# Performance work log

Measured on AMD Instinct MI355X. Metric: run time of the kernel, lower is better.

Reference implementation:

```python
import jax, jax.numpy as jnp
import numpy as np

NUM_THETAS = 64   # bump_steps == num_thetas == 64
NUM_PTS = 100
B = 256           # number of graphs
N = B * NUM_PTS   # total nodes
SCALE = 500.0     # sigmoid sharpness used by EctLayer
HID = 4 * 1024


def _linear_init(key, fan_in, shape):
    s = 1.0 / np.sqrt(fan_in)
    return jax.random.uniform(key, shape, jnp.float32, -s, s)


def setup_inputs() -> dict:
    key = jax.random.key(0)
    ks = jax.random.split(key, 8)
    x = jax.random.normal(ks[0], (N, 2), jnp.float32)
    batch_idx = jnp.repeat(jnp.arange(B), NUM_PTS)  # [N] graph id per node
    t = jnp.linspace(0.0, 2.0 * np.pi, NUM_THETAS)
    V = jnp.stack([jnp.sin(t), jnp.cos(t)], axis=0)          # [2, T] directions
    lin = jnp.linspace(-1.0, 1.0, NUM_THETAS)                # [bump] thresholds
    d = NUM_THETAS * NUM_THETAS
    W1 = _linear_init(ks[1], d, (d, HID)); b1 = _linear_init(ks[2], d, (HID,))
    W2 = _linear_init(ks[3], HID, (HID, HID)); b2 = _linear_init(ks[4], HID, (HID,))
    W3 = _linear_init(ks[5], HID, (HID, 2 * NUM_PTS)); b3 = _linear_init(ks[6], HID, (2 * NUM_PTS,))
    return {"x": x, "batch_idx": batch_idx, "V": V, "lin": lin,
            "W1": W1, "b1": b1, "W2": W2, "b2": b2, "W3": W3, "b3": b3}


def ect_layer(x, idx, V, lin, num_graphs):
    # x: [N,2], V: [2,T] -> node heights nh: [N,T]
    nh = x @ V
    # soft-threshold binning: [N, bump, T]
    ecc = jax.nn.sigmoid(SCALE * (lin[None, :, None] - nh[:, None, :]))
    # per-graph scatter-sum over nodes -> [B, bump, T]
    e = jax.ops.segment_sum(ecc, idx, num_segments=num_graphs)
    # normalized=True: divide by per-graph max
    return e / jnp.amax(e, axis=(1, 2), keepdims=True)


def reference(x, batch_idx, V, lin, W1, b1, W2, b2, W3, b3):
    ect = ect_layer(x, batch_idx, V, lin, B)          # [B, 64, 64]
    h = ect.reshape(B, -1)                            # Flatten
    h = jnp.tanh(h @ W1 + b1)
    h = jnp.tanh(h @ W2 + b2)
    pts = (h @ W3 + b3).reshape(-1, 2)                # [B*NUM_PTS, 2]
    idx2 = jnp.repeat(jnp.arange(B), NUM_PTS)
    decoded = ect_layer(pts, idx2, V, lin, B)         # [B, 64, 64]
    return decoded, pts
```

## Files before the change

### kernel.cpp

```cpp
#include <hip/hip_runtime.h>
#include <hip/hip_bf16.h>

typedef short bf16x8 __attribute__((ext_vector_type(8)));
typedef short s16x4 __attribute__((ext_vector_type(4)));
typedef float f32x4 __attribute__((ext_vector_type(4)));
typedef unsigned u32x4 __attribute__((ext_vector_type(4)));

#define ECT_SCALE 500.0f

__device__ __forceinline__ bool detect_f32(const void* w) {
    const unsigned* p = (const unsigned*)w;
    int sane = 0;
#pragma unroll
    for (int i = 0; i < 16; i++) {
        unsigned e = (p[i] >> 7) & 0xFFu;
        sane += (e >= 100u && e <= 140u) ? 1 : 0;
    }
    return sane < 10;
}

__device__ __forceinline__ float ld_f(const void* p, int i, bool f32) {
    return f32 ? ((const float*)p)[i]
               : __bfloat162float(((const __hip_bfloat16*)p)[i]);
}

__device__ __forceinline__ void split_f(float v, short& hi, short& lo) {
    __hip_bfloat16 h = __float2bfloat16(v);
    hi = (short)__bfloat16_as_short(h);
    lo = (short)__bfloat16_as_short(__float2bfloat16(v - __bfloat162float(h)));
}

__device__ __forceinline__ float sig_fast(float x) {
    float t = __builtin_amdgcn_fmed3f(x, 0.0f, 1.0f);
    return t * t * (3.0f - 2.0f * t);
}

__global__ __launch_bounds__(512)
void ect1_kernel(const void* __restrict__ x, const void* __restrict__ V,
                 const void* __restrict__ lin, const void* __restrict__ sent,
                 short* __restrict__ eh, short* __restrict__ el)
{
    __shared__ float in_lds[200];
    __shared__ float nh[100 * 64];
    __shared__ float wmax[8];

    const bool f32 = detect_f32(sent);
    const int g = blockIdx.x, tid = threadIdx.x;
    const int t = tid & 63, wv = tid >> 6;

    if (tid < 200) in_lds[tid] = ld_f(x, g * 200 + tid, f32);
    const float sv = ld_f(V, t, f32);
    const float cv = ld_f(V, 64 + t, f32);
    float zs[8];
#pragma unroll
    for (int k = 0; k < 8; k++)
        zs[k] = (ECT_SCALE / 8.0f) * ld_f(lin, wv + 8 * k, f32) + 0.5f;
    __syncthreads();

    for (int n = wv; n < 100; n += 8)
        nh[n * 64 + t] = in_lds[2 * n] * sv + in_lds[2 * n + 1] * cv;

    float e[8];
#pragma unroll
    for (int k = 0; k < 8; k++) e[k] = 0.0f;
    __syncthreads();

    for (int n = 0; n < 100; n++) {
        const float ws = (ECT_SCALE / 8.0f) * nh[n * 64 + t];
#pragma unroll
        for (int k = 0; k < 8; k++)
            e[k] += sig_fast(zs[k] - ws);
    }

    float mx = e[0];
#pragma unroll
    for (int k = 1; k < 8; k++) mx = fmaxf(mx, e[k]);
#pragma unroll
    for (int off = 32; off > 0; off >>= 1)
        mx = fmaxf(mx, __shfl_xor(mx, off, 64));
    if (t == 0) wmax[wv] = mx;
    __syncthreads();
    float gm = wmax[0];
#pragma unroll
    for (int k = 1; k < 8; k++) gm = fmaxf(gm, wmax[k]);
    const float sc = 1.0f / gm;

#pragma unroll
    for (int k = 0; k < 8; k++) {
        short hi, lo;
        split_f(e[k] * sc, hi, lo);
        eh[g * 4096 + tid + 512 * k] = hi;
        el[g * 4096 + tid + 512 * k] = lo;
    }
}

#define PREFETCH(k0_)                                                          \
    {                                                                          \
        _Pragma("unroll")                                                      \
        for (int p = 0; p < 2; p++) {                                          \
            int r = ar + 64 * p;                                               \
            pah[p] = *(const bf16x8*)&Ah[(size_t)(bm * 128 + r) * 4096 + (k0_) + ac]; \
            pal[p] = *(const bf16x8*)&Al[(size_t)(bm * 128 + r) * 4096 + (k0_) + ac]; \
        }                                                                      \
        _Pragma("unroll")                                                      \
        for (int c = 0; c < 2; c++)                                            \
            _Pragma("unroll")                                                  \
            for (int j = 0; j < 8; j++) {                                      \
                size_t off = (size_t)((k0_) + wk + j) * 4096 + n0c + lane + 64 * c; \
                pw[c * 8 + j] = f32 ? ((const unsigned*)W)[off]                \
                                    : ((unsigned)((const unsigned short*)W)[off] << 16); \
            }                                                                  \
    }

__global__ __launch_bounds__(256)
void gemm128(const short* __restrict__ Ah, const short* __restrict__ Al,
             const void* __restrict__ W, const void* __restrict__ sent,
             float* __restrict__ pre)
{
    __shared__ short Ahs[128][40], Als[128][40], Bhs[128][40], Bls[128][40];
    const bool f32 = detect_f32(sent);
    const int bm = blockIdx.y;
    const int bn = blockIdx.x >> 3;
    const int kz = blockIdx.x & 7;
    const int tid = threadIdx.x;
    const int wv = tid >> 6, lane = tid & 63, quad = lane >> 4, l16 = lane & 15;
    const int wm = (wv & 1) * 64, wn = (wv >> 1) * 64;
    const int ar = tid >> 2, ac = (tid & 3) * 8;
    const int n0c = bn * 128;
    const int wk = wv * 8;

    f32x4 acc[4][4];
#pragma unroll
    for (int i = 0; i < 4; i++)
#pragma unroll
        for (int j = 0; j < 4; j++) acc[i][j] = (f32x4){0.f, 0.f, 0.f, 0.f};

    bf16x8 pah[2], pal[2];
    unsigned pw[16];

    const int k0base = kz * 512;
    PREFETCH(k0base)

    for (int it = 0; it < 16; it++) {
#pragma unroll
        for (int p = 0; p < 2; p++) {
            *(bf16x8*)&Ahs[ar + 64 * p][ac] = pah[p];
            *(bf16x8*)&Als[ar + 64 * p][ac] = pal[p];
        }
#pragma unroll
        for (int c = 0; c < 2; c++) {
            unsigned hp[4], lp[4];
#pragma unroll
            for (int jp = 0; jp < 4; jp++) {
                unsigned a = pw[c * 8 + 2 * jp], b = pw[c * 8 + 2 * jp + 1];
                unsigned ha = a & 0xFFFF0000u, hb = b & 0xFFFF0000u;
                hp[jp] = (ha >> 16) | hb;
                float la = __uint_as_float(a) - __uint_as_float(ha);
                float lb = __uint_as_float(b) - __uint_as_float(hb);
                lp[jp] = (__float_as_uint(la) >> 16) |
                         (__float_as_uint(lb) & 0xFFFF0000u);
            }
            *(u32x4*)&Bhs[lane + 64 * c][wk] = (u32x4){hp[0], hp[1], hp[2], hp[3]};
            *(u32x4*)&Bls[lane + 64 * c][wk] = (u32x4){lp[0], lp[1], lp[2], lp[3]};
        }
        __syncthreads();

        if (it < 15) PREFETCH(k0base + (it + 1) * 32)

        bf16x8 ahf[4], alf[4];
#pragma unroll
        for (int i = 0; i < 4; i++) {
            ahf[i] = *(const bf16x8*)&Ahs[wm + i * 16 + l16][quad * 8];
            alf[i] = *(const bf16x8*)&Als[wm + i * 16 + l16][quad * 8];
        }
#pragma unroll
        for (int j = 0; j < 4; j++) {
            bf16x8 bh = *(const bf16x8*)&Bhs[wn + j * 16 + l16][quad * 8];
            bf16x8 bl = *(const bf16x8*)&Bls[wn + j * 16 + l16][quad * 8];
#pragma unroll
            for (int i = 0; i < 4; i++) {
                acc[i][j] = __builtin_amdgcn_mfma_f32_16x16x32_bf16(ahf[i], bh, acc[i][j], 0, 0, 0);
                acc[i][j] = __builtin_amdgcn_mfma_f32_16x16x32_bf16(ahf[i], bl, acc[i][j], 0, 0, 0);
                acc[i][j] = __builtin_amdgcn_mfma_f32_16x16x32_bf16(alf[i], bh, acc[i][j], 0, 0, 0);
            }
        }
        __syncthreads();
    }

    float* ps = pre + (size_t)kz * (256 * 4096);
#pragma unroll
    for (int i = 0; i < 4; i++)
#pragma unroll
        for (int j = 0; j < 4; j++) {
            const int n = n0c + wn + j * 16 + l16;
#pragma unroll
            for (int r = 0; r < 4; r++) {
                const int m = bm * 128 + wm + i * 16 + quad * 4 + r;
                ps[(size_t)m * 4096 + n] = acc[i][j][r];
            }
        }
}

__global__ __launch_bounds__(256)
void finalize8(const float* __restrict__ pre, const void* __restrict__ bias,
               const void* __restrict__ sent,
               short* __restrict__ Oh, short* __restrict__ Ol)
{
    const bool f32 = detect_f32(sent);
    const int idx = (blockIdx.x * 256 + threadIdx.x) * 4;
    f32x4 s = (f32x4){0.f, 0.f, 0.f, 0.f};
#pragma unroll
    for (int z = 0; z < 8; z++)
        s += *(const f32x4*)&pre[(size_t)z * 1048576 + idx];
    const int n = idx & 4095;
    s16x4 hi, lo;
#pragma unroll
    for (int j = 0; j < 4; j++) {
        float t = s[j] + ld_f(bias, n + j, f32);
        t = 1.0f - 2.0f * __builtin_amdgcn_rcpf(1.0f + __expf(2.0f * t));
        short h, l;
        split_f(t, h, l);
        hi[j] = h; lo[j] = l;
    }
    *(s16x4*)&Oh[idx] = hi;
    *(s16x4*)&Ol[idx] = lo;
}

__global__ __launch_bounds__(256)
void gemm_sk3(const short* __restrict__ Ah, const short* __restrict__ Al,
              const void* __restrict__ W, const void* __restrict__ sent,
              float* __restrict__ part)
{
    __shared__ short Ahs[64][72], Als[64][72], Bhs[64][72], Bls[64][72];
    const bool f32 = detect_f32(sent);
    const int N_ = 200, K_ = 4096;
    const int bm = blockIdx.y;
    const int bn = blockIdx.x >> 5;
    const int kz = blockIdx.x & 31;
    const int tid = threadIdx.x;
    const int wv = tid >> 6, lane = tid & 63, quad = lane >> 4, l16 = lane & 15;
    const int mrow0 = (wv & 1) * 32, ncol0 = (wv >> 1) * 32;
    const int rr = tid >> 3, cc = (tid & 7) * 8;
    const int n0c = bn * 64;

    f32x4 acc[2][2];
#pragma unroll
    for (int i = 0; i < 2; i++)
#pragma unroll
        for (int j = 0; j < 2; j++) acc[i][j] = (f32x4){0.f, 0.f, 0.f, 0.f};

    int k0 = kz * 128;
    for (int it = 0; it < 2; it++, k0 += 64) {
#pragma unroll
        for (int i = 0; i < 2; i++) {
            int r = rr + 32 * i;
            *(bf16x8*)&Ahs[r][cc] = *(const bf16x8*)&Ah[(size_t)(bm * 64 + r) * K_ + k0 + cc];
            *(bf16x8*)&Als[r][cc] = *(const bf16x8*)&Al[(size_t)(bm * 64 + r) * K_ + k0 + cc];
        }
        {
            const int wn2 = lane, wk2 = wv * 16;
            const bool okn = (n0c + wn2 < N_);
            unsigned pw2[16];
#pragma unroll
            for (int j = 0; j < 16; j++) {
                size_t off = (size_t)(k0 + wk2 + j) * N_ + n0c + wn2;
                pw2[j] = !okn ? 0u
                       : (f32 ? ((const unsigned*)W)[off]
                              : ((unsigned)((const unsigned short*)W)[off] << 16));
            }
            unsigned hp[8], lp[8];
#pragma unroll
            for (int jp = 0; jp < 8; jp++) {
                unsigned a = pw2[2 * jp], b = pw2[2 * jp + 1];
                unsigned ha = a & 0xFFFF0000u, hb = b & 0xFFFF0000u;
                hp[jp] = (ha >> 16) | hb;
                float la = __uint_as_float(a) - __uint_as_float(ha);
                float lb = __uint_as_float(b) - __uint_as_float(hb);
                lp[jp] = (__float_as_uint(la) >> 16) | (__float_as_uint(lb) & 0xFFFF0000u);
            }
            *(u32x4*)&Bhs[wn2][wk2]     = (u32x4){hp[0], hp[1], hp[2], hp[3]};
            *(u32x4*)&Bhs[wn2][wk2 + 8] = (u32x4){hp[4], hp[5], hp[6], hp[7]};
            *(u32x4*)&Bls[wn2][wk2]     = (u32x4){lp[0], lp[1], lp[2], lp[3]};
            *(u32x4*)&Bls[wn2][wk2 + 8] = (u32x4){lp[4], lp[5], lp[6], lp[7]};
        }
        __syncthreads();
#pragma unroll
        for (int kh = 0; kh < 2; kh++) {
            bf16x8 ah2[2], al2[2];
#pragma unroll
            for (int im = 0; im < 2; im++) {
                ah2[im] = *(const bf16x8*)&Ahs[mrow0 + im * 16 + l16][kh * 32 + quad * 8];
                al2[im] = *(const bf16x8*)&Als[mrow0 + im * 16 + l16][kh * 32 + quad * 8];
            }
#pragma unroll
            for (int jn = 0; jn < 2; jn++) {
                bf16x8 bh = *(const bf16x8*)&Bhs[ncol0 + jn * 16 + l16][kh * 32 + quad * 8];
                bf16x8 bl = *(const bf16x8*)&Bls[ncol0 + jn * 16 + l16][kh * 32 + quad * 8];
#pragma unroll
                for (int im = 0; im < 2; im++) {
                    acc[im][jn] = __builtin_amdgcn_mfma_f32_16x16x32_bf16(ah2[im], bh, acc[im][jn], 0, 0, 0);
                    acc[im][jn] = __builtin_amdgcn_mfma_f32_16x16x32_bf16(ah2[im], bl, acc[im][jn], 0, 0, 0);
                    acc[im][jn] = __builtin_amdgcn_mfma_f32_16x16x32_bf16(al2[im], bh, acc[im][jn], 0, 0, 0);
                }
            }
        }
        __syncthreads();
    }

    float* ps = part + (size_t)kz * (256 * 200);
#pragma unroll
    for (int im = 0; im < 2; im++)
#pragma unroll
        for (int jn = 0; jn < 2; jn++) {
            const int n = n0c + ncol0 + jn * 16 + l16;
            if (n < N_) {
#pragma unroll
                for (int r = 0; r < 4; r++) {
                    const int m = bm * 64 + mrow0 + im * 16 + quad * 4 + r;
                    ps[m * 200 + n] = acc[im][jn][r];
                }
            }
        }
}

__global__ __launch_bounds__(512)
void ect2_kernel(const float* __restrict__ part, const void* __restrict__ bias3,
                 const void* __restrict__ V, const void* __restrict__ lin,
                 const void* __restrict__ sent,
                 float* __restrict__ dec, float* __restrict__ pts_out)
{
    __shared__ float in_lds[200];
    __shared__ float nh[100 * 64];
    __shared__ float wmax[8];

    const bool f32 = detect_f32(sent);
    const int g = blockIdx.x, tid = threadIdx.x;
    const int t = tid & 63, wv = tid >> 6;

    if (tid < 200) {
        float v = ld_f(bias3, tid, f32);
#pragma unroll
        for (int z = 0; z < 32; z++)
            v += part[(size_t)z * 51200 + g * 200 + tid];
        in_lds[tid] = v;
        pts_out[g * 200 + tid] = v;
    }
    const float sv = ld_f(V, t, f32);
    const float cv = ld_f(V, 64 + t, f32);
    float zs[8];
#pragma unroll
    for (int k = 0; k < 8; k++)
        zs[k] = (ECT_SCALE / 8.0f) * ld_f(lin, wv + 8 * k, f32) + 0.5f;
    __syncthreads();

    for (int n = wv; n < 100; n += 8)
        nh[n * 64 + t] = in_lds[2 * n] * sv + in_lds[2 * n + 1] * cv;

    float e[8];
#pragma unroll
    for (int k = 0; k < 8; k++) e[k] = 0.0f;
    __syncthreads();

    for (int n = 0; n < 100; n++) {
        const float ws = (ECT_SCALE / 8.0f) * nh[n * 64 + t];
#pragma unroll
        for (int k = 0; k < 8; k++)
            e[k] += sig_fast(zs[k] - ws);
    }

    float mx = e[0];
#pragma unroll
    for (int k = 1; k < 8; k++) mx = fmaxf(mx, e[k]);
#pragma unroll
    for (int off = 32; off > 0; off >>= 1)
        mx = fmaxf(mx, __shfl_xor(mx, off, 64));
    if (t == 0) wmax[wv] = mx;
    __syncthreads();
    float gm = wmax[0];
#pragma unroll
    for (int k = 1; k < 8; k++) gm = fmaxf(gm, wmax[k]);
    const float sc = 1.0f / gm;

#pragma unroll
    for (int k = 0; k < 8; k++)
        dec[g * 4096 + tid + 512 * k] = e[k] * sc;
}

extern "C" void kernel_launch(void* const* d_in, const int* in_sizes, int n_in,
                              void* d_out, int out_size, void* d_ws, size_t ws_size,
                              hipStream_t stream)
{
    const void* x   = d_in[0];
    const void* V   = d_in[2];
    const void* lin = d_in[3];
    const void* W1  = d_in[4];
    const void* b1  = d_in[5];
    const void* W2  = d_in[6];
    const void* b2  = d_in[7];
    const void* W3  = d_in[8];
    const void* b3  = d_in[9];
    float* out = (float*)d_out;

    char* ws = (char*)d_ws;
    short* e_h  = (short*)(ws + ( 0u << 20));
    short* e_l  = (short*)(ws + ( 2u << 20));
    short* h1h  = (short*)(ws + ( 4u << 20));
    short* h1l  = (short*)(ws + ( 6u << 20));
    short* h2h  = (short*)(ws + ( 8u << 20));
    short* h2l  = (short*)(ws + (10u << 20));
    float* pre  = (float*)(ws + (12u << 20));
    float* part = (float*)(ws + (44u << 20));

    ect1_kernel<<<256, 512, 0, stream>>>(x, V, lin, W1, e_h, e_l);
    gemm128<<<dim3(256, 2), 256, 0, stream>>>(e_h, e_l, W1, W1, pre);
    finalize8<<<1024, 256, 0, stream>>>(pre, b1, W1, h1h, h1l);
    gemm128<<<dim3(256, 2), 256, 0, stream>>>(h1h, h1l, W2, W1, pre);
    finalize8<<<1024, 256, 0, stream>>>(pre, b2, W1, h2h, h2l);
    gemm_sk3<<<dim3(128, 4), 256, 0, stream>>>(h2h, h2l, W3, W1, part);
    ect2_kernel<<<256, 512, 0, stream>>>(part, b3, V, lin, W1, out, out + 1048576);
}
```

Baseline: 268.9 us.

## Shrink gemm128 N-tile to 64, swizzle B LDS, skip low-part MFMAs for bf16 weights

The gemm128 N-tile drops from 128 to 64 columns and the grid doubles, so more blocks are resident (launch bounds now request 4 per CU) and each wave holds fewer accumulators. B-tile LDS writes and reads use an XOR swizzle to cut bank conflicts. Pointer-increment prefetching replaces recomputed offsets. When the weights are bf16, the low-part B split and its MFMA are skipped in both GEMM kernels, since that part is zero. The smaller tile means less reuse of each loaded A tile and more global traffic for A.

```diff
diff --git a/kernel.cpp b/kernel.cpp
--- a/kernel.cpp
+++ b/kernel.cpp
@@ -94,109 +94,132 @@
     }
 }
 
-#define PREFETCH(k0_)                                                          \
+#define STAGE_PF()                                                             \
     {                                                                          \
-        _Pragma("unroll")                                                      \
-        for (int p = 0; p < 2; p++) {                                          \
-            int r = ar + 64 * p;                                               \
-            pah[p] = *(const bf16x8*)&Ah[(size_t)(bm * 128 + r) * 4096 + (k0_) + ac]; \
-            pal[p] = *(const bf16x8*)&Al[(size_t)(bm * 128 + r) * 4096 + (k0_) + ac]; \
+        pah[0] = *(const bf16x8*)a0; pah[1] = *(const bf16x8*)a1;              \
+        pal[0] = *(const bf16x8*)l0; pal[1] = *(const bf16x8*)l1;              \
+        if (f32) {                                                             \
+            _Pragma("unroll")                                                  \
+            for (int j = 0; j < 8; j++)                                        \
+                pw[j] = *(const unsigned*)(wp + (size_t)j * wrow);             \
+        } else {                                                               \
+            _Pragma("unroll")                                                  \
+            for (int j = 0; j < 8; j++)                                        \
+                pw[j] = (unsigned)(*(const unsigned short*)(wp + (size_t)j * wrow)) << 16; \
         }                                                                      \
-        _Pragma("unroll")                                                      \
-        for (int c = 0; c < 2; c++)                                            \
-            _Pragma("unroll")                                                  \
-            for (int j = 0; j < 8; j++) {                                      \
-                size_t off = (size_t)((k0_) + wk + j) * 4096 + n0c + lane + 64 * c; \
-                pw[c * 8 + j] = f32 ? ((const unsigned*)W)[off]                \
-                                    : ((unsigned)((const unsigned short*)W)[off] << 16); \
-            }                                                                  \
-    }
-
-__global__ __launch_bounds__(256)
+        a0 += 32; a1 += 32; l0 += 32; l1 += 32; wp += 32 * wrow;               \
+    }
+
+__global__ __launch_bounds__(256, 4)
 void gemm128(const short* __restrict__ Ah, const short* __restrict__ Al,
              const void* __restrict__ W, const void* __restrict__ sent,
              float* __restrict__ pre)
 {
-    __shared__ short Ahs[128][40], Als[128][40], Bhs[128][40], Bls[128][40];
+    __shared__ short Ahs[128][40], Als[128][40], Bhs[64][40], Bls[64][40];
     const bool f32 = detect_f32(sent);
     const int bm = blockIdx.y;
     const int bn = blockIdx.x >> 3;
     const int kz = blockIdx.x & 7;
     const int tid = threadIdx.x;
     const int wv = tid >> 6, lane = tid & 63, quad = lane >> 4, l16 = lane & 15;
-    const int wm = (wv & 1) * 64, wn = (wv >> 1) * 64;
+    const int wm = wv * 32;
     const int ar = tid >> 2, ac = (tid & 3) * 8;
-    const int n0c = bn * 128;
+    const int n0c = bn * 64;
     const int wk = wv * 8;
-
-    f32x4 acc[4][4];
-#pragma unroll
-    for (int i = 0; i < 4; i++)
+    const int bwcol = (wv ^ ((lane >> 3) & 3)) * 8;
+
+    f32x4 acc[2][4];
+#pragma unroll
+    for (int i = 0; i < 2; i++)
 #pragma unroll
         for (int j = 0; j < 4; j++) acc[i][j] = (f32x4){0.f, 0.f, 0.f, 0.f};
 
     bf16x8 pah[2], pal[2];
-    unsigned pw[16];
-
-    const int k0base = kz * 512;
-    PREFETCH(k0base)
+    unsigned pw[8];
+
+    const size_t welt = f32 ? 4u : 2u;
+    const size_t wrow = (size_t)4096 * welt;
+    const char* wp = (const char*)W + ((size_t)(kz * 512 + wk) * 4096 + (n0c + lane)) * welt;
+    const short* a0 = Ah + (size_t)(bm * 128 + ar) * 4096 + kz * 512 + ac;
+    const short* a1 = a0 + (size_t)64 * 4096;
+    const short* l0 = Al + (size_t)(bm * 128 + ar) * 4096 + kz * 512 + ac;
+    const short* l1 = l0 + (size_t)64 * 4096;
+
+    STAGE_PF()
 
     for (int it = 0; it < 16; it++) {
-#pragma unroll
-        for (int p = 0; p < 2; p++) {
-            *(bf16x8*)&Ahs[ar + 64 * p][ac] = pah[p];
-            *(bf16x8*)&Als[ar + 64 * p][ac] = pal[p];
-        }
-#pragma unroll
-        for (int c = 0; c < 2; c++) {
+        *(bf16x8*)&Ahs[ar][ac]      = pah[0];
+        *(bf16x8*)&Ahs[ar + 64][ac] = pah[1];
+        *(bf16x8*)&Als[ar][ac]      = pal[0];
+        *(bf16x8*)&Als[ar + 64][ac] = pal[1];
+        {
             unsigned hp[4], lp[4];
 #pragma unroll
             for (int jp = 0; jp < 4; jp++) {
-                unsigned a = pw[c * 8 + 2 * jp], b = pw[c * 8 + 2 * jp + 1];
+                unsigned a = pw[2 * jp], b = pw[2 * jp + 1];
                 unsigned ha = a & 0xFFFF0000u, hb = b & 0xFFFF0000u;
                 hp[jp] = (ha >> 16) | hb;
-                float la = __uint_as_float(a) - __uint_as_float(ha);
-                float lb = __uint_as_float(b) - __uint_as_float(hb);
-                lp[jp] = (__float_as_uint(la) >> 16) |
-                         (__float_as_uint(lb) & 0xFFFF0000u);
-            }
-            *(u32x4*)&Bhs[lane + 64 * c][wk] = (u32x4){hp[0], hp[1], hp[2], hp[3]};
-            *(u32x4*)&Bls[lane + 64 * c][wk] = (u32x4){lp[0], lp[1], lp[2], lp[3]};
+                if (f32) {
+                    float la = __uint_as_float(a) - __uint_as_float(ha);
+                    float lb = __uint_as_float(b) - __uint_as_float(hb);
+                    lp[jp] = (__float_as_uint(la) >> 16) |
+                             (__float_as_uint(lb) & 0xFFFF0000u);
+                }
+            }
+            *(u32x4*)&Bhs[lane][bwcol] = (u32x4){hp[0], hp[1], hp[2], hp[3]};
+            if (f32)
+                *(u32x4*)&Bls[lane][bwcol] = (u32x4){lp[0], lp[1], lp[2], lp[3]};
         }
         __syncthreads();
 
-        if (it < 15) PREFETCH(k0base + (it + 1) * 32)
-
-        bf16x8 ahf[4], alf[4];
-#pragma unroll
-        for (int i = 0; i < 4; i++) {
-            ahf[i] = *(const bf16x8*)&Ahs[wm + i * 16 + l16][quad * 8];
-            alf[i] = *(const bf16x8*)&Als[wm + i * 16 + l16][quad * 8];
-        }
+        if (it < 15) STAGE_PF()
+
+        bf16x8 ahf[2], alf[2];
+#pragma unroll
+        for (int im = 0; im < 2; im++) {
+            ahf[im] = *(const bf16x8*)&Ahs[wm + im * 16 + l16][quad * 8];
+            alf[im] = *(const bf16x8*)&Als[wm + im * 16 + l16][quad * 8];
+        }
+        if (f32) {
+#pragma unroll
+            for (int j = 0; j < 4; j++) {
+                const int br = j * 16 + l16;
+                const int bc = (quad ^ ((br >> 3) & 3)) * 8;
+                bf16x8 bh = *(const bf16x8*)&Bhs[br][bc];
+                bf16x8 bl = *(const bf16x8*)&Bls[br][bc];
+#pragma unroll
+                for (int im = 0; im < 2; im++) {
+                    acc[im][j] = __builtin_amdgcn_mfma_f32_16x16x32_bf16(ahf[im], bh, acc[im][j], 0, 0, 0);
+                    acc[im][j] = __builtin_amdgcn_mfma_f32_16x16x32_bf16(ahf[im], bl, acc[im][j], 0, 0, 0);
+                    acc[im][j] = __builtin_amdgcn_mfma_f32_16x16x32_bf16(alf[im], bh, acc[im][j], 0, 0, 0);
+                }
+            }
+        } else {
+#pragma unroll
+            for (int j = 0; j < 4; j++) {
+                const int br = j * 16 + l16;
+                const int bc = (quad ^ ((br >> 3) & 3)) * 8;
+                bf16x8 bh = *(const bf16x8*)&Bhs[br][bc];
+#pragma unroll
+                for (int im = 0; im < 2; im++) {
+                    acc[im][j] = __builtin_amdgcn_mfma_f32_16x16x32_bf16(ahf[im], bh, acc[im][j], 0, 0, 0);
+                    acc[im][j] = __builtin_amdgcn_mfma_f32_16x16x32_bf16(alf[im], bh, acc[im][j], 0, 0, 0);
+                }
+            }
+        }
+        __syncthreads();
+    }
+
+    float* ps = pre + (size_t)kz * (256 * 4096);
+#pragma unroll
+    for (int im = 0; im < 2; im++)
 #pragma unroll
         for (int j = 0; j < 4; j++) {
-            bf16x8 bh = *(const bf16x8*)&Bhs[wn + j * 16 + l16][quad * 8];
-            bf16x8 bl = *(const bf16x8*)&Bls[wn + j * 16 + l16][quad * 8];
-#pragma unroll
-            for (int i = 0; i < 4; i++) {
-                acc[i][j] = __builtin_amdgcn_mfma_f32_16x16x32_bf16(ahf[i], bh, acc[i][j], 0, 0, 0);
-                acc[i][j] = __builtin_amdgcn_mfma_f32_16x16x32_bf16(ahf[i], bl, acc[i][j], 0, 0, 0);
-                acc[i][j] = __builtin_amdgcn_mfma_f32_16x16x32_bf16(alf[i], bh, acc[i][j], 0, 0, 0);
-            }
-        }
-        __syncthreads();
-    }
-
-    float* ps = pre + (size_t)kz * (256 * 4096);
-#pragma unroll
-    for (int i = 0; i < 4; i++)
-#pragma unroll
-        for (int j = 0; j < 4; j++) {
-            const int n = n0c + wn + j * 16 + l16;
+            const int n = n0c + j * 16 + l16;
 #pragma unroll
             for (int r = 0; r < 4; r++) {
-                const int m = bm * 128 + wm + i * 16 + quad * 4 + r;
-                ps[(size_t)m * 4096 + n] = acc[i][j][r];
+                const int m = bm * 128 + wm + im * 16 + quad * 4 + r;
+                ps[(size_t)m * 4096 + n] = acc[im][j][r];
             }
         }
 }
@@ -274,14 +297,18 @@
                 unsigned a = pw2[2 * jp], b = pw2[2 * jp + 1];
                 unsigned ha = a & 0xFFFF0000u, hb = b & 0xFFFF0000u;
                 hp[jp] = (ha >> 16) | hb;
-                float la = __uint_as_float(a) - __uint_as_float(ha);
-                float lb = __uint_as_float(b) - __uint_as_float(hb);
-                lp[jp] = (__float_as_uint(la) >> 16) | (__float_as_uint(lb) & 0xFFFF0000u);
+                if (f32) {
+                    float la = __uint_as_float(a) - __uint_as_float(ha);
+                    float lb = __uint_as_float(b) - __uint_as_float(hb);
+                    lp[jp] = (__float_as_uint(la) >> 16) | (__float_as_uint(lb) & 0xFFFF0000u);
+                }
             }
             *(u32x4*)&Bhs[wn2][wk2]     = (u32x4){hp[0], hp[1], hp[2], hp[3]};
             *(u32x4*)&Bhs[wn2][wk2 + 8] = (u32x4){hp[4], hp[5], hp[6], hp[7]};
-            *(u32x4*)&Bls[wn2][wk2]     = (u32x4){lp[0], lp[1], lp[2], lp[3]};
-            *(u32x4*)&Bls[wn2][wk2 + 8] = (u32x4){lp[4], lp[5], lp[6], lp[7]};
+            if (f32) {
+                *(u32x4*)&Bls[wn2][wk2]     = (u32x4){lp[0], lp[1], lp[2], lp[3]};
+                *(u32x4*)&Bls[wn2][wk2 + 8] = (u32x4){lp[4], lp[5], lp[6], lp[7]};
+            }
         }
         __syncthreads();
 #pragma unroll
@@ -292,15 +319,27 @@
                 ah2[im] = *(const bf16x8*)&Ahs[mrow0 + im * 16 + l16][kh * 32 + quad * 8];
                 al2[im] = *(const bf16x8*)&Als[mrow0 + im * 16 + l16][kh * 32 + quad * 8];
             }
-#pragma unroll
-            for (int jn = 0; jn < 2; jn++) {
-                bf16x8 bh = *(const bf16x8*)&Bhs[ncol0 + jn * 16 + l16][kh * 32 + quad * 8];
-                bf16x8 bl = *(const bf16x8*)&Bls[ncol0 + jn * 16 + l16][kh * 32 + quad * 8];
-#pragma unroll
-                for (int im = 0; im < 2; im++) {
-                    acc[im][jn] = __builtin_amdgcn_mfma_f32_16x16x32_bf16(ah2[im], bh, acc[im][jn], 0, 0, 0);
-                    acc[im][jn] = __builtin_amdgcn_mfma_f32_16x16x32_bf16(ah2[im], bl, acc[im][jn], 0, 0, 0);
-                    acc[im][jn] = __builtin_amdgcn_mfma_f32_16x16x32_bf16(al2[im], bh, acc[im][jn], 0, 0, 0);
+            if (f32) {
+#pragma unroll
+                for (int jn = 0; jn < 2; jn++) {
+                    bf16x8 bh = *(const bf16x8*)&Bhs[ncol0 + jn * 16 + l16][kh * 32 + quad * 8];
+                    bf16x8 bl = *(const bf16x8*)&Bls[ncol0 + jn * 16 + l16][kh * 32 + quad * 8];
+#pragma unroll
+                    for (int im = 0; im < 2; im++) {
+                        acc[im][jn] = __builtin_amdgcn_mfma_f32_16x16x32_bf16(ah2[im], bh, acc[im][jn], 0, 0, 0);
+                        acc[im][jn] = __builtin_amdgcn_mfma_f32_16x16x32_bf16(ah2[im], bl, acc[im][jn], 0, 0, 0);
+                        acc[im][jn] = __builtin_amdgcn_mfma_f32_16x16x32_bf16(al2[im], bh, acc[im][jn], 0, 0, 0);
+                    }
+                }
+            } else {
+#pragma unroll
+                for (int jn = 0; jn < 2; jn++) {
+                    bf16x8 bh = *(const bf16x8*)&Bhs[ncol0 + jn * 16 + l16][kh * 32 + quad * 8];
+#pragma unroll
+                    for (int im = 0; im < 2; im++) {
+                        acc[im][jn] = __builtin_amdgcn_mfma_f32_16x16x32_bf16(ah2[im], bh, acc[im][jn], 0, 0, 0);
+                        acc[im][jn] = __builtin_amdgcn_mfma_f32_16x16x32_bf16(al2[im], bh, acc[im][jn], 0, 0, 0);
+                    }
                 }
             }
         }
@@ -412,9 +451,9 @@
     float* part = (float*)(ws + (44u << 20));
 
     ect1_kernel<<<256, 512, 0, stream>>>(x, V, lin, W1, e_h, e_l);
-    gemm128<<<dim3(256, 2), 256, 0, stream>>>(e_h, e_l, W1, W1, pre);
+    gemm128<<<dim3(512, 2), 256, 0, stream>>>(e_h, e_l, W1, W1, pre);
     finalize8<<<1024, 256, 0, stream>>>(pre, b1, W1, h1h, h1l);
-    gemm128<<<dim3(256, 2), 256, 0, stream>>>(h1h, h1l, W2, W1, pre);
+    gemm128<<<dim3(512, 2), 256, 0, stream>>>(h1h, h1l, W2, W1, pre);
     finalize8<<<1024, 256, 0, stream>>>(pre, b2, W1, h2h, h2l);
     gemm_sk3<<<dim3(128, 4), 256, 0, stream>>>(h2h, h2l, W3, W1, part);
     ect2_kernel<<<256, 512, 0, stream>>>(part, b3, V, lin, W1, out, out + 1048576);
```

Result: slower. 278.5 us (+3.6%).

## Double-buffer GEMM prefetch registers and skip low-part MFMA for bf16 weights

Applied to the files above, without the earlier changes.

The main GEMM now keeps two register prefetch sets, so global loads are issued two K-steps ahead, and it walks incrementing pointers instead of recomputing addresses each step. Launch bounds ask for two blocks per CU. When the weights are detected as bf16, the low-half split, its shared-memory store and the third MFMA product are skipped in both the main GEMM and the output GEMM, because the low half is zero in that case. The cost is higher register pressure from the doubled prefetch buffers and the occupancy hint, which could cause spills.

```diff
diff --git a/kernel.cpp b/kernel.cpp
--- a/kernel.cpp
+++ b/kernel.cpp
@@ -94,25 +94,86 @@
     }
 }
 
-#define PREFETCH(k0_)                                                          \
+#define PFSET(S)                                                               \
     {                                                                          \
-        _Pragma("unroll")                                                      \
-        for (int p = 0; p < 2; p++) {                                          \
-            int r = ar + 64 * p;                                               \
-            pah[p] = *(const bf16x8*)&Ah[(size_t)(bm * 128 + r) * 4096 + (k0_) + ac]; \
-            pal[p] = *(const bf16x8*)&Al[(size_t)(bm * 128 + r) * 4096 + (k0_) + ac]; \
-        }                                                                      \
-        _Pragma("unroll")                                                      \
-        for (int c = 0; c < 2; c++)                                            \
+        pah##S[0] = *(const bf16x8*)a0; pah##S[1] = *(const bf16x8*)a1;        \
+        pal##S[0] = *(const bf16x8*)l0; pal##S[1] = *(const bf16x8*)l1;        \
+        if (f32) {                                                             \
             _Pragma("unroll")                                                  \
             for (int j = 0; j < 8; j++) {                                      \
-                size_t off = (size_t)((k0_) + wk + j) * 4096 + n0c + lane + 64 * c; \
-                pw[c * 8 + j] = f32 ? ((const unsigned*)W)[off]                \
-                                    : ((unsigned)((const unsigned short*)W)[off] << 16); \
+                pw##S[j]     = *(const unsigned*)(wp + (size_t)j * wrow);      \
+                pw##S[8 + j] = *(const unsigned*)(wp + (size_t)j * wrow + 256);\
             }                                                                  \
-    }
-
-__global__ __launch_bounds__(256)
+        } else {                                                               \
+            _Pragma("unroll")                                                  \
+            for (int j = 0; j < 8; j++) {                                      \
+                pw##S[j]     = (unsigned)(*(const unsigned short*)(wp + (size_t)j * wrow)) << 16; \
+                pw##S[8 + j] = (unsigned)(*(const unsigned short*)(wp + (size_t)j * wrow + 128)) << 16; \
+            }                                                                  \
+        }                                                                      \
+        a0 += 32; a1 += 32; l0 += 32; l1 += 32; wp += 32 * wrow;               \
+    }
+
+#define GBODY(S, IT)                                                           \
+    {                                                                          \
+        *(bf16x8*)&Ahs[ar][ac]      = pah##S[0];                               \
+        *(bf16x8*)&Ahs[ar + 64][ac] = pah##S[1];                               \
+        *(bf16x8*)&Als[ar][ac]      = pal##S[0];                               \
+        *(bf16x8*)&Als[ar + 64][ac] = pal##S[1];                               \
+        _Pragma("unroll")                                                      \
+        for (int c = 0; c < 2; c++) {                                          \
+            unsigned hp[4], lp[4];                                             \
+            _Pragma("unroll")                                                  \
+            for (int jp = 0; jp < 4; jp++) {                                   \
+                unsigned a = pw##S[c * 8 + 2 * jp], b = pw##S[c * 8 + 2 * jp + 1]; \
+                unsigned ha = a & 0xFFFF0000u, hb = b & 0xFFFF0000u;           \
+                hp[jp] = (ha >> 16) | hb;                                      \
+                if (f32) {                                                     \
+                    float la = __uint_as_float(a) - __uint_as_float(ha);       \
+                    float lb = __uint_as_float(b) - __uint_as_float(hb);       \
+                    lp[jp] = (__float_as_uint(la) >> 16) |                     \
+                             (__float_as_uint(lb) & 0xFFFF0000u);              \
+                }                                                              \
+            }                                                                  \
+            *(u32x4*)&Bhs[lane + 64 * c][wk] = (u32x4){hp[0], hp[1], hp[2], hp[3]}; \
+            if (f32)                                                           \
+                *(u32x4*)&Bls[lane + 64 * c][wk] = (u32x4){lp[0], lp[1], lp[2], lp[3]}; \
+        }                                                                      \
+        __syncthreads();                                                       \
+        if ((IT) + 2 < 16) PFSET(S)                                            \
+        bf16x8 ahf[4], alf[4];                                                 \
+        _Pragma("unroll")                                                      \
+        for (int i = 0; i < 4; i++) {                                          \
+            ahf[i] = *(const bf16x8*)&Ahs[wm + i * 16 + l16][quad * 8];        \
+            alf[i] = *(const bf16x8*)&Als[wm + i * 16 + l16][quad * 8];        \
+        }                                                                      \
+        if (f32) {                                                             \
+            _Pragma("unroll")                                                  \
+            for (int j = 0; j < 4; j++) {                                      \
+                bf16x8 bh = *(const bf16x8*)&Bhs[wn + j * 16 + l16][quad * 8]; \
+                bf16x8 bl = *(const bf16x8*)&Bls[wn + j * 16 + l16][quad * 8]; \
+                _Pragma("unroll")                                              \
+                for (int i = 0; i < 4; i++) {                                  \
+                    acc[i][j] = __builtin_amdgcn_mfma_f32_16x16x32_bf16(ahf[i], bh, acc[i][j], 0, 0, 0); \
+                    acc[i][j] = __builtin_amdgcn_mfma_f32_16x16x32_bf16(ahf[i], bl, acc[i][j], 0, 0, 0); \
+                    acc[i][j] = __builtin_amdgcn_mfma_f32_16x16x32_bf16(alf[i], bh, acc[i][j], 0, 0, 0); \
+                }                                                              \
+            }                                                                  \
+        } else {                                                               \
+            _Pragma("unroll")                                                  \
+            for (int j = 0; j < 4; j++) {                                      \
+                bf16x8 bh = *(const bf16x8*)&Bhs[wn + j * 16 + l16][quad * 8]; \
+                _Pragma("unroll")                                              \
+                for (int i = 0; i < 4; i++) {                                  \
+                    acc[i][j] = __builtin_amdgcn_mfma_f32_16x16x32_bf16(ahf[i], bh, acc[i][j], 0, 0, 0); \
+                    acc[i][j] = __builtin_amdgcn_mfma_f32_16x16x32_bf16(alf[i], bh, acc[i][j], 0, 0, 0); \
+                }                                                              \
+            }                                                                  \
+        }                                                                      \
+        __syncthreads();                                                       \
+    }
+
+__global__ __launch_bounds__(256, 2)
 void gemm128(const short* __restrict__ Ah, const short* __restrict__ Al,
              const void* __restrict__ W, const void* __restrict__ sent,
              float* __restrict__ pre)
@@ -135,56 +196,23 @@
 #pragma unroll
         for (int j = 0; j < 4; j++) acc[i][j] = (f32x4){0.f, 0.f, 0.f, 0.f};
 
-    bf16x8 pah[2], pal[2];
-    unsigned pw[16];
-
-    const int k0base = kz * 512;
-    PREFETCH(k0base)
-
-    for (int it = 0; it < 16; it++) {
-#pragma unroll
-        for (int p = 0; p < 2; p++) {
-            *(bf16x8*)&Ahs[ar + 64 * p][ac] = pah[p];
-            *(bf16x8*)&Als[ar + 64 * p][ac] = pal[p];
-        }
-#pragma unroll
-        for (int c = 0; c < 2; c++) {
-            unsigned hp[4], lp[4];
-#pragma unroll
-            for (int jp = 0; jp < 4; jp++) {
-                unsigned a = pw[c * 8 + 2 * jp], b = pw[c * 8 + 2 * jp + 1];
-                unsigned ha = a & 0xFFFF0000u, hb = b & 0xFFFF0000u;
-                hp[jp] = (ha >> 16) | hb;
-                float la = __uint_as_float(a) - __uint_as_float(ha);
-                float lb = __uint_as_float(b) - __uint_as_float(hb);
-                lp[jp] = (__float_as_uint(la) >> 16) |
-                         (__float_as_uint(lb) & 0xFFFF0000u);
-            }
-            *(u32x4*)&Bhs[lane + 64 * c][wk] = (u32x4){hp[0], hp[1], hp[2], hp[3]};
-            *(u32x4*)&Bls[lane + 64 * c][wk] = (u32x4){lp[0], lp[1], lp[2], lp[3]};
-        }
-        __syncthreads();
-
-        if (it < 15) PREFETCH(k0base + (it + 1) * 32)
-
-        bf16x8 ahf[4], alf[4];
-#pragma unroll
-        for (int i = 0; i < 4; i++) {
-            ahf[i] = *(const bf16x8*)&Ahs[wm + i * 16 + l16][quad * 8];
-            alf[i] = *(const bf16x8*)&Als[wm + i * 16 + l16][quad * 8];
-        }
-#pragma unroll
-        for (int j = 0; j < 4; j++) {
-            bf16x8 bh = *(const bf16x8*)&Bhs[wn + j * 16 + l16][quad * 8];
-            bf16x8 bl = *(const bf16x8*)&Bls[wn + j * 16 + l16][quad * 8];
-#pragma unroll
-            for (int i = 0; i < 4; i++) {
-                acc[i][j] = __builtin_amdgcn_mfma_f32_16x16x32_bf16(ahf[i], bh, acc[i][j], 0, 0, 0);
-                acc[i][j] = __builtin_amdgcn_mfma_f32_16x16x32_bf16(ahf[i], bl, acc[i][j], 0, 0, 0);
-                acc[i][j] = __builtin_amdgcn_mfma_f32_16x16x32_bf16(alf[i], bh, acc[i][j], 0, 0, 0);
-            }
-        }
-        __syncthreads();
+    bf16x8 pah0[2], pal0[2], pah1[2], pal1[2];
+    unsigned pw0[16], pw1[16];
+
+    const size_t welt = f32 ? 4u : 2u;
+    const size_t wrow = (size_t)4096 * welt;
+    const char* wp = (const char*)W + ((size_t)(kz * 512 + wk) * 4096 + (n0c + lane)) * welt;
+    const short* a0 = Ah + (size_t)(bm * 128 + ar) * 4096 + kz * 512 + ac;
+    const short* a1 = a0 + (size_t)64 * 4096;
+    const short* l0 = Al + (size_t)(bm * 128 + ar) * 4096 + kz * 512 + ac;
+    const short* l1 = l0 + (size_t)64 * 4096;
+
+    PFSET(0)
+    PFSET(1)
+
+    for (int itp = 0; itp < 8; itp++) {
+        GBODY(0, 2 * itp)
+        GBODY(1, 2 * itp + 1)
     }
 
     float* ps = pre + (size_t)kz * (256 * 4096);
@@ -274,14 +302,18 @@
                 unsigned a = pw2[2 * jp], b = pw2[2 * jp + 1];
                 unsigned ha = a & 0xFFFF0000u, hb = b & 0xFFFF0000u;
                 hp[jp] = (ha >> 16) | hb;
-                float la = __uint_as_float(a) - __uint_as_float(ha);
-                float lb = __uint_as_float(b) - __uint_as_float(hb);
-                lp[jp] = (__float_as_uint(la) >> 16) | (__float_as_uint(lb) & 0xFFFF0000u);
+                if (f32) {
+                    float la = __uint_as_float(a) - __uint_as_float(ha);
+                    float lb = __uint_as_float(b) - __uint_as_float(hb);
+                    lp[jp] = (__float_as_uint(la) >> 16) | (__float_as_uint(lb) & 0xFFFF0000u);
+                }
             }
             *(u32x4*)&Bhs[wn2][wk2]     = (u32x4){hp[0], hp[1], hp[2], hp[3]};
             *(u32x4*)&Bhs[wn2][wk2 + 8] = (u32x4){hp[4], hp[5], hp[6], hp[7]};
-            *(u32x4*)&Bls[wn2][wk2]     = (u32x4){lp[0], lp[1], lp[2], lp[3]};
-            *(u32x4*)&Bls[wn2][wk2 + 8] = (u32x4){lp[4], lp[5], lp[6], lp[7]};
+            if (f32) {
+                *(u32x4*)&Bls[wn2][wk2]     = (u32x4){lp[0], lp[1], lp[2], lp[3]};
+                *(u32x4*)&Bls[wn2][wk2 + 8] = (u32x4){lp[4], lp[5], lp[6], lp[7]};
+            }
         }
         __syncthreads();
 #pragma unroll
@@ -292,15 +324,27 @@
                 ah2[im] = *(const bf16x8*)&Ahs[mrow0 + im * 16 + l16][kh * 32 + quad * 8];
                 al2[im] = *(const bf16x8*)&Als[mrow0 + im * 16 + l16][kh * 32 + quad * 8];
             }
-#pragma unroll
-            for (int jn = 0; jn < 2; jn++) {
-                bf16x8 bh = *(const bf16x8*)&Bhs[ncol0 + jn * 16 + l16][kh * 32 + quad * 8];
-                bf16x8 bl = *(const bf16x8*)&Bls[ncol0 + jn * 16 + l16][kh * 32 + quad * 8];
-#pragma unroll
-                for (int im = 0; im < 2; im++) {
-                    acc[im][jn] = __builtin_amdgcn_mfma_f32_16x16x32_bf16(ah2[im], bh, acc[im][jn], 0, 0, 0);
-                    acc[im][jn] = __builtin_amdgcn_mfma_f32_16x16x32_bf16(ah2[im], bl, acc[im][jn], 0, 0, 0);
-                    acc[im][jn] = __builtin_amdgcn_mfma_f32_16x16x32_bf16(al2[im], bh, acc[im][jn], 0, 0, 0);
+            if (f32) {
+#pragma unroll
+                for (int jn = 0; jn < 2; jn++) {
+                    bf16x8 bh = *(const bf16x8*)&Bhs[ncol0 + jn * 16 + l16][kh * 32 + quad * 8];
+                    bf16x8 bl = *(const bf16x8*)&Bls[ncol0 + jn * 16 + l16][kh * 32 + quad * 8];
+#pragma unroll
+                    for (int im = 0; im < 2; im++) {
+                        acc[im][jn] = __builtin_amdgcn_mfma_f32_16x16x32_bf16(ah2[im], bh, acc[im][jn], 0, 0, 0);
+                        acc[im][jn] = __builtin_amdgcn_mfma_f32_16x16x32_bf16(ah2[im], bl, acc[im][jn], 0, 0, 0);
+                        acc[im][jn] = __builtin_amdgcn_mfma_f32_16x16x32_bf16(al2[im], bh, acc[im][jn], 0, 0, 0);
+                    }
+                }
+            } else {
+#pragma unroll
+                for (int jn = 0; jn < 2; jn++) {
+                    bf16x8 bh = *(const bf16x8*)&Bhs[ncol0 + jn * 16 + l16][kh * 32 + quad * 8];
+#pragma unroll
+                    for (int im = 0; im < 2; im++) {
+                        acc[im][jn] = __builtin_amdgcn_mfma_f32_16x16x32_bf16(ah2[im], bh, acc[im][jn], 0, 0, 0);
+                        acc[im][jn] = __builtin_amdgcn_mfma_f32_16x16x32_bf16(al2[im], bh, acc[im][jn], 0, 0, 0);
+                    }
                 }
             }
         }
```

Result: no change. 269.3 us (+0.2%).

## Double K-tile depth in gemm128 and skip low-part MFMAs for bf16 weights

Applied to the files above, without the earlier changes.

The main split-K GEMM now stages 64-wide K tiles instead of 32, halving the number of loop iterations and barriers. Global loads use pointer increments instead of recomputed offsets, and occupancy is hinted with launch_bounds(256,2). When the weights are detected as bf16, the low-part split of W is skipped along with one of three MFMAs per tile in both GEMM kernels. The cost is larger LDS use, more prefetch registers, and a hand-written end-of-iteration barrier with an explicit lgkmcnt wait.

```diff
diff --git a/kernel.cpp b/kernel.cpp
--- a/kernel.cpp
+++ b/kernel.cpp
@@ -94,30 +94,35 @@
     }
 }
 
-#define PREFETCH(k0_)                                                          \
+#define PFSET()                                                                \
     {                                                                          \
         _Pragma("unroll")                                                      \
-        for (int p = 0; p < 2; p++) {                                          \
-            int r = ar + 64 * p;                                               \
-            pah[p] = *(const bf16x8*)&Ah[(size_t)(bm * 128 + r) * 4096 + (k0_) + ac]; \
-            pal[p] = *(const bf16x8*)&Al[(size_t)(bm * 128 + r) * 4096 + (k0_) + ac]; \
+        for (int p = 0; p < 4; p++) {                                          \
+            pah[p] = *(const bf16x8*)(a0 + 8 * p);                             \
+            pal[p] = *(const bf16x8*)(l0 + 8 * p);                             \
         }                                                                      \
-        _Pragma("unroll")                                                      \
-        for (int c = 0; c < 2; c++)                                            \
+        if (f32) {                                                             \
             _Pragma("unroll")                                                  \
-            for (int j = 0; j < 8; j++) {                                      \
-                size_t off = (size_t)((k0_) + wk + j) * 4096 + n0c + lane + 64 * c; \
-                pw[c * 8 + j] = f32 ? ((const unsigned*)W)[off]                \
-                                    : ((unsigned)((const unsigned short*)W)[off] << 16); \
+            for (int j = 0; j < 16; j++) {                                     \
+                pw[j]      = *(const unsigned*)(wp + (size_t)j * wrow);        \
+                pw[16 + j] = *(const unsigned*)(wp + (size_t)j * wrow + 256);  \
             }                                                                  \
-    }
-
-__global__ __launch_bounds__(256)
+        } else {                                                               \
+            _Pragma("unroll")                                                  \
+            for (int j = 0; j < 16; j++) {                                     \
+                pw[j]      = (unsigned)(*(const unsigned short*)(wp + (size_t)j * wrow)) << 16; \
+                pw[16 + j] = (unsigned)(*(const unsigned short*)(wp + (size_t)j * wrow + 128)) << 16; \
+            }                                                                  \
+        }                                                                      \
+        a0 += 64; l0 += 64; wp += 64 * wrow;                                   \
+    }
+
+__global__ __launch_bounds__(256, 2)
 void gemm128(const short* __restrict__ Ah, const short* __restrict__ Al,
              const void* __restrict__ W, const void* __restrict__ sent,
              float* __restrict__ pre)
 {
-    __shared__ short Ahs[128][40], Als[128][40], Bhs[128][40], Bls[128][40];
+    __shared__ short Ahs[128][72], Als[128][72], Bhs[128][72], Bls[128][72];
     const bool f32 = detect_f32(sent);
     const int bm = blockIdx.y;
     const int bn = blockIdx.x >> 3;
@@ -125,9 +130,9 @@
     const int tid = threadIdx.x;
     const int wv = tid >> 6, lane = tid & 63, quad = lane >> 4, l16 = lane & 15;
     const int wm = (wv & 1) * 64, wn = (wv >> 1) * 64;
-    const int ar = tid >> 2, ac = (tid & 3) * 8;
+    const int ar = tid >> 1, ac = (tid & 1) * 32;
     const int n0c = bn * 128;
-    const int wk = wv * 8;
+    const int wk = wv * 16;
 
     f32x4 acc[4][4];
 #pragma unroll
@@ -135,56 +140,85 @@
 #pragma unroll
         for (int j = 0; j < 4; j++) acc[i][j] = (f32x4){0.f, 0.f, 0.f, 0.f};
 
-    bf16x8 pah[2], pal[2];
-    unsigned pw[16];
-
-    const int k0base = kz * 512;
-    PREFETCH(k0base)
-
-    for (int it = 0; it < 16; it++) {
-#pragma unroll
-        for (int p = 0; p < 2; p++) {
-            *(bf16x8*)&Ahs[ar + 64 * p][ac] = pah[p];
-            *(bf16x8*)&Als[ar + 64 * p][ac] = pal[p];
+    bf16x8 pah[4], pal[4];
+    unsigned pw[32];
+
+    const size_t welt = f32 ? 4u : 2u;
+    const size_t wrow = (size_t)4096 * welt;
+    const char* wp = (const char*)W + ((size_t)(kz * 512 + wk) * 4096 + (n0c + lane)) * welt;
+    const short* a0 = Ah + (size_t)(bm * 128 + ar) * 4096 + kz * 512 + ac;
+    const short* l0 = Al + (size_t)(bm * 128 + ar) * 4096 + kz * 512 + ac;
+
+    PFSET()
+
+    for (int it = 0; it < 8; it++) {
+#pragma unroll
+        for (int p = 0; p < 4; p++) {
+            *(bf16x8*)&Ahs[ar][ac + 8 * p] = pah[p];
+            *(bf16x8*)&Als[ar][ac + 8 * p] = pal[p];
         }
 #pragma unroll
         for (int c = 0; c < 2; c++) {
-            unsigned hp[4], lp[4];
-#pragma unroll
-            for (int jp = 0; jp < 4; jp++) {
-                unsigned a = pw[c * 8 + 2 * jp], b = pw[c * 8 + 2 * jp + 1];
+            unsigned hp[8], lp[8];
+#pragma unroll
+            for (int jp = 0; jp < 8; jp++) {
+                unsigned a = pw[c * 16 + 2 * jp], b = pw[c * 16 + 2 * jp + 1];
                 unsigned ha = a & 0xFFFF0000u, hb = b & 0xFFFF0000u;
                 hp[jp] = (ha >> 16) | hb;
-                float la = __uint_as_float(a) - __uint_as_float(ha);
-                float lb = __uint_as_float(b) - __uint_as_float(hb);
-                lp[jp] = (__float_as_uint(la) >> 16) |
-                         (__float_as_uint(lb) & 0xFFFF0000u);
-            }
-            *(u32x4*)&Bhs[lane + 64 * c][wk] = (u32x4){hp[0], hp[1], hp[2], hp[3]};
-            *(u32x4*)&Bls[lane + 64 * c][wk] = (u32x4){lp[0], lp[1], lp[2], lp[3]};
+                if (f32) {
+                    float la = __uint_as_float(a) - __uint_as_float(ha);
+                    float lb = __uint_as_float(b) - __uint_as_float(hb);
+                    lp[jp] = (__float_as_uint(la) >> 16) |
+                             (__float_as_uint(lb) & 0xFFFF0000u);
+                }
+            }
+            *(u32x4*)&Bhs[lane + 64 * c][wk]     = (u32x4){hp[0], hp[1], hp[2], hp[3]};
+            *(u32x4*)&Bhs[lane + 64 * c][wk + 8] = (u32x4){hp[4], hp[5], hp[6], hp[7]};
+            if (f32) {
+                *(u32x4*)&Bls[lane + 64 * c][wk]     = (u32x4){lp[0], lp[1], lp[2], lp[3]};
+                *(u32x4*)&Bls[lane + 64 * c][wk + 8] = (u32x4){lp[4], lp[5], lp[6], lp[7]};
+            }
         }
         __syncthreads();
 
-        if (it < 15) PREFETCH(k0base + (it + 1) * 32)
-
-        bf16x8 ahf[4], alf[4];
-#pragma unroll
-        for (int i = 0; i < 4; i++) {
-            ahf[i] = *(const bf16x8*)&Ahs[wm + i * 16 + l16][quad * 8];
-            alf[i] = *(const bf16x8*)&Als[wm + i * 16 + l16][quad * 8];
-        }
-#pragma unroll
-        for (int j = 0; j < 4; j++) {
-            bf16x8 bh = *(const bf16x8*)&Bhs[wn + j * 16 + l16][quad * 8];
-            bf16x8 bl = *(const bf16x8*)&Bls[wn + j * 16 + l16][quad * 8];
+        if (it < 7) PFSET()
+
+#pragma unroll
+        for (int kk = 0; kk < 2; kk++) {
+            bf16x8 ahf[4], alf[4];
 #pragma unroll
             for (int i = 0; i < 4; i++) {
-                acc[i][j] = __builtin_amdgcn_mfma_f32_16x16x32_bf16(ahf[i], bh, acc[i][j], 0, 0, 0);
-                acc[i][j] = __builtin_amdgcn_mfma_f32_16x16x32_bf16(ahf[i], bl, acc[i][j], 0, 0, 0);
-                acc[i][j] = __builtin_amdgcn_mfma_f32_16x16x32_bf16(alf[i], bh, acc[i][j], 0, 0, 0);
-            }
-        }
-        __syncthreads();
+                ahf[i] = *(const bf16x8*)&Ahs[wm + i * 16 + l16][kk * 32 + quad * 8];
+                alf[i] = *(const bf16x8*)&Als[wm + i * 16 + l16][kk * 32 + quad * 8];
+            }
+            if (f32) {
+#pragma unroll
+                for (int j = 0; j < 4; j++) {
+                    bf16x8 bh = *(const bf16x8*)&Bhs[wn + j * 16 + l16][kk * 32 + quad * 8];
+                    bf16x8 bl = *(const bf16x8*)&Bls[wn + j * 16 + l16][kk * 32 + quad * 8];
+#pragma unroll
+                    for (int i = 0; i < 4; i++) {
+                        acc[i][j] = __builtin_amdgcn_mfma_f32_16x16x32_bf16(ahf[i], bh, acc[i][j], 0, 0, 0);
+                        acc[i][j] = __builtin_amdgcn_mfma_f32_16x16x32_bf16(ahf[i], bl, acc[i][j], 0, 0, 0);
+                        acc[i][j] = __builtin_amdgcn_mfma_f32_16x16x32_bf16(alf[i], bh, acc[i][j], 0, 0, 0);
+                    }
+                }
+            } else {
+#pragma unroll
+                for (int j = 0; j < 4; j++) {
+                    bf16x8 bh = *(const bf16x8*)&Bhs[wn + j * 16 + l16][kk * 32 + quad * 8];
+#pragma unroll
+                    for (int i = 0; i < 4; i++) {
+                        acc[i][j] = __builtin_amdgcn_mfma_f32_16x16x32_bf16(ahf[i], bh, acc[i][j], 0, 0, 0);
+                        acc[i][j] = __builtin_amdgcn_mfma_f32_16x16x32_bf16(alf[i], bh, acc[i][j], 0, 0, 0);
+                    }
+                }
+            }
+        }
+
+        asm volatile("s_waitcnt lgkmcnt(0)" ::: "memory");
+        __builtin_amdgcn_s_barrier();
+        asm volatile("" ::: "memory");
     }
 
     float* ps = pre + (size_t)kz * (256 * 4096);
@@ -274,14 +308,18 @@
                 unsigned a = pw2[2 * jp], b = pw2[2 * jp + 1];
                 unsigned ha = a & 0xFFFF0000u, hb = b & 0xFFFF0000u;
                 hp[jp] = (ha >> 16) | hb;
-                float la = __uint_as_float(a) - __uint_as_float(ha);
-                float lb = __uint_as_float(b) - __uint_as_float(hb);
-                lp[jp] = (__float_as_uint(la) >> 16) | (__float_as_uint(lb) & 0xFFFF0000u);
+                if (f32) {
+                    float la = __uint_as_float(a) - __uint_as_float(ha);
+                    float lb = __uint_as_float(b) - __uint_as_float(hb);
+                    lp[jp] = (__float_as_uint(la) >> 16) | (__float_as_uint(lb) & 0xFFFF0000u);
+                }
             }
             *(u32x4*)&Bhs[wn2][wk2]     = (u32x4){hp[0], hp[1], hp[2], hp[3]};
             *(u32x4*)&Bhs[wn2][wk2 + 8] = (u32x4){hp[4], hp[5], hp[6], hp[7]};
-            *(u32x4*)&Bls[wn2][wk2]     = (u32x4){lp[0], lp[1], lp[2], lp[3]};
-            *(u32x4*)&Bls[wn2][wk2 + 8] = (u32x4){lp[4], lp[5], lp[6], lp[7]};
+            if (f32) {
+                *(u32x4*)&Bls[wn2][wk2]     = (u32x4){lp[0], lp[1], lp[2], lp[3]};
+                *(u32x4*)&Bls[wn2][wk2 + 8] = (u32x4){lp[4], lp[5], lp[6], lp[7]};
+            }
         }
         __syncthreads();
 #pragma unroll
@@ -292,15 +330,27 @@
                 ah2[im] = *(const bf16x8*)&Ahs[mrow0 + im * 16 + l16][kh * 32 + quad * 8];
                 al2[im] = *(const bf16x8*)&Als[mrow0 + im * 16 + l16][kh * 32 + quad * 8];
             }
-#pragma unroll
-            for (int jn = 0; jn < 2; jn++) {
-                bf16x8 bh = *(const bf16x8*)&Bhs[ncol0 + jn * 16 + l16][kh * 32 + quad * 8];
-                bf16x8 bl = *(const bf16x8*)&Bls[ncol0 + jn * 16 + l16][kh * 32 + quad * 8];
-#pragma unroll
-                for (int im = 0; im < 2; im++) {
-                    acc[im][jn] = __builtin_amdgcn_mfma_f32_16x16x32_bf16(ah2[im], bh, acc[im][jn], 0, 0, 0);
-                    acc[im][jn] = __builtin_amdgcn_mfma_f32_16x16x32_bf16(ah2[im], bl, acc[im][jn], 0, 0, 0);
-                    acc[im][jn] = __builtin_amdgcn_mfma_f32_16x16x32_bf16(al2[im], bh, acc[im][jn], 0, 0, 0);
+            if (f32) {
+#pragma unroll
+                for (int jn = 0; jn < 2; jn++) {
+                    bf16x8 bh = *(const bf16x8*)&Bhs[ncol0 + jn * 16 + l16][kh * 32 + quad * 8];
+                    bf16x8 bl = *(const bf16x8*)&Bls[ncol0 + jn * 16 + l16][kh * 32 + quad * 8];
+#pragma unroll
+                    for (int im = 0; im < 2; im++) {
+                        acc[im][jn] = __builtin_amdgcn_mfma_f32_16x16x32_bf16(ah2[im], bh, acc[im][jn], 0, 0, 0);
+                        acc[im][jn] = __builtin_amdgcn_mfma_f32_16x16x32_bf16(ah2[im], bl, acc[im][jn], 0, 0, 0);
+                        acc[im][jn] = __builtin_amdgcn_mfma_f32_16x16x32_bf16(al2[im], bh, acc[im][jn], 0, 0, 0);
+                    }
+                }
+            } else {
+#pragma unroll
+                for (int jn = 0; jn < 2; jn++) {
+                    bf16x8 bh = *(const bf16x8*)&Bhs[ncol0 + jn * 16 + l16][kh * 32 + quad * 8];
+#pragma unroll
+                    for (int im = 0; im < 2; im++) {
+                        acc[im][jn] = __builtin_amdgcn_mfma_f32_16x16x32_bf16(ah2[im], bh, acc[im][jn], 0, 0, 0);
+                        acc[im][jn] = __builtin_amdgcn_mfma_f32_16x16x32_bf16(al2[im], bh, acc[im][jn], 0, 0, 0);
+                    }
                 }
             }
         }
```

Measured after the change: 255.8 us. 4.9% less time.
